# Performance work log

Hardware: AMD Instinct MI355X
Metric: run time of the kernel (lower is better)

## Reference

```python
import jax, jax.numpy as jnp
import numpy as np

DIM = 512
HEADS = 8
SCALE = (DIM // HEADS) ** -0.5  # 0.125
B, H, W = 1, 64, 64  # square spatial grid required by torch matmul broadcasting


def setup_inputs() -> dict:
    key = jax.random.key(0)
    ks = jax.random.split(key, 7)
    s = DIM ** -0.5
    return {
        "x": jax.random.normal(ks[0], (B, H, W, DIM), dtype=jnp.float32),
        "mask": 0,  # sentinel for None (mask must be None in the original)
        "Wq": jax.random.normal(ks[1], (DIM, DIM), dtype=jnp.float32) * s,
        "bq": jax.random.normal(ks[2], (DIM,), dtype=jnp.float32) * 0.01,
        "Wk": jax.random.normal(ks[3], (DIM, DIM), dtype=jnp.float32) * s,
        "bk": jax.random.normal(ks[4], (DIM,), dtype=jnp.float32) * 0.01,
        "Wv": jax.random.normal(ks[5], (DIM, DIM), dtype=jnp.float32) * s,
        "bv": jax.random.normal(ks[6], (DIM,), dtype=jnp.float32) * 0.01,
    }


def reference(x, mask, Wq, bq, Wk, bk, Wv, bv):
    # Linear projections (nn.Linear: x @ W.T + b)
    q = jnp.einsum('bhwc,oc->bhwo', x, Wq) + bq
    k = jnp.einsum('bhwc,oc->bhwo', x, Wk) + bk
    v = jnp.einsum('bhwc,oc->bhwo', x, Wv) + bv
    # Faithful to torch.einsum('bhwc,bpqd->bhwpq', q, k): c and d are each
    # summed independently => outer product of channel-sums. [b,h,w,p,q]
    weights = jnp.einsum('bhwc,bpqd->bhwpq', q, k)
    # dropout is identity in eval mode; then scale and softmax over last axis
    weights = jax.nn.softmax(weights * SCALE, axis=-1)
    # torch matmul broadcasting: [b,h,w,p,q] @ [b,p,q,d] -> [b,h,w,p,d]
    attn = jnp.matmul(weights, v)
    return attn
```

## Files before the change

### kernel.cpp

```cpp
#include <hip/hip_runtime.h>

typedef _Float16 half8 __attribute__((ext_vector_type(8)));
typedef float f32x4 __attribute__((ext_vector_type(4)));
typedef float float4_t __attribute__((ext_vector_type(4)));
typedef unsigned int uint32x2 __attribute__((ext_vector_type(2)));

#define DIM 512
#define S 64
#define NROW 4096
#define LDSW 88

__global__ void colsum2_kernel(const float* __restrict__ Wq, const float* __restrict__ bq,
                               const float* __restrict__ Wk, const float* __restrict__ bk,
                               float* __restrict__ wsumq, float* __restrict__ wsumk) {
    int sel = blockIdx.x >> 5;
    int b = blockIdx.x & 31;
    const float* W = sel ? Wk : Wq;
    const float* bias = sel ? bk : bq;
    float* wsum = sel ? wsumk : wsumq;
    int t = threadIdx.x;
    int c0 = t, c1 = t + 256;
    float s0 = 0.f, s1 = 0.f;
    const float* Wr = W + (size_t)b * 16 * DIM;
#pragma unroll
    for (int o = 0; o < 16; ++o) {
        s0 += Wr[o * DIM + c0];
        s1 += Wr[o * DIM + c1];
    }
    atomicAdd(&wsum[c0], s0);
    atomicAdd(&wsum[c1], s1);
    if (b == 0) {
        float bs = bias[c0] + bias[c1];
#pragma unroll
        for (int off = 32; off >= 1; off >>= 1) bs += __shfl_xor(bs, off);
        if ((t & 63) == 0) atomicAdd(&wsum[512], bs);
    }
}

__global__ void rowdot_kernel(const float* __restrict__ X,
                              const float* __restrict__ wqsum,
                              const float* __restrict__ wksum,
                              float* __restrict__ a_arr,
                              float* __restrict__ ks_arr) {
    int wave = threadIdx.x >> 6;
    int lane = threadIdx.x & 63;
    int row = blockIdx.x * 4 + wave;
    const float4_t* xr = (const float4_t*)(X + (size_t)row * DIM) + lane * 2;
    const float4_t* wq = (const float4_t*)wqsum + lane * 2;
    const float4_t* wk = (const float4_t*)wksum + lane * 2;
    float4_t x0 = xr[0], x1 = xr[1];
    float4_t q0 = wq[0], q1 = wq[1];
    float4_t k0 = wk[0], k1 = wk[1];
    float sq = 0.f, sk = 0.f;
#pragma unroll
    for (int i = 0; i < 4; i++) {
        sq += x0[i] * q0[i] + x1[i] * q1[i];
        sk += x0[i] * k0[i] + x1[i] * k1[i];
    }
#pragma unroll
    for (int off = 32; off >= 1; off >>= 1) {
        sq += __shfl_xor(sq, off);
        sk += __shfl_xor(sk, off);
    }
    if (lane == 0) {
        a_arr[row]  = (sq + wqsum[DIM]) * 0.125f;
        ks_arr[row] = sk + wksum[DIM];
    }
}

__global__ void vt_gemm_kernel(const float* __restrict__ X,
                               const float* __restrict__ Wv,
                               const float* __restrict__ bv,
                               _Float16* __restrict__ Vs) {
    int mb = blockIdx.x;
    int cb = blockIdx.y;
    int wv_ = threadIdx.x >> 6;
    int lane = threadIdx.x & 63;
    int lr = lane & 15;
    int lg = lane >> 4;
    int row0 = mb * 16;
    int col0 = cb * 256 + wv_ * 64;

    f32x4 acc[4];
#pragma unroll
    for (int n = 0; n < 4; n++) acc[n] = (f32x4){0.f, 0.f, 0.f, 0.f};

    for (int kk = 0; kk < 16; ++kk) {
        int kbase = kk * 32 + lg * 8;
        const float4_t* pa = (const float4_t*)(X + (size_t)(row0 + lr) * DIM + kbase);
        float4_t x0 = pa[0], x1 = pa[1];
        half8 a;
#pragma unroll
        for (int i = 0; i < 4; i++) { a[i] = (_Float16)x0[i]; a[i + 4] = (_Float16)x1[i]; }
#pragma unroll
        for (int n = 0; n < 4; n++) {
            const float4_t* pb = (const float4_t*)(Wv + (size_t)(col0 + n * 16 + lr) * DIM + kbase);
            float4_t b0 = pb[0], b1 = pb[1];
            half8 hb;
#pragma unroll
            for (int i = 0; i < 4; i++) { hb[i] = (_Float16)b0[i]; hb[i + 4] = (_Float16)b1[i]; }
            acc[n] = __builtin_amdgcn_mfma_f32_16x16x32_f16(a, hb, acc[n], 0, 0, 0);
        }
    }
    int w   = mb >> 2;
    int s_  = (mb & 3) >> 1;
    int lg2 = ((mb & 3) * 2 + (lg >> 1)) & 3;
    int e0  = (lg & 1) * 4;
#pragma unroll
    for (int n = 0; n < 4; n++) {
        int d = col0 + n * 16 + lr;
        int dt = d >> 4;
        float bvc = bv[d];
        _Float16 tmp[4];
#pragma unroll
        for (int r = 0; r < 4; r++) tmp[r] = (_Float16)(acc[n][r] + bvc);
        int idx8 = (((w * 32 + dt) * 2 + s_) * 4 + lg2) * 16 + lr;
        __builtin_nontemporal_store(*(uint32x2*)tmp, (uint32x2*)(Vs + (size_t)idx8 * 8 + e0));
    }
}

__global__ __launch_bounds__(256) void attn_main_kernel(
        const float* __restrict__ a_arr,
        const float* __restrict__ ks_arr,
        const _Float16* __restrict__ Vs,
        float* __restrict__ out) {
    __shared__ _Float16 Wsm[64 * LDSW];
    __shared__ float Osm[64 * 128];
    int hw = blockIdx.x;
    int w = hw & 63;
    int t = threadIdx.x;
    int wv_ = t >> 6, lane = t & 63;
    int lr = lane & 15, lg = lane >> 4;

    float a = a_arr[hw];

    {
        int p = t >> 2, c = t & 3;
        const float4_t* kp = (const float4_t*)(ks_arr + p * 64 + c * 16);
        float4_t k0 = kp[0], k1 = kp[1], k2 = kp[2], k3 = kp[3];
        float L[16];
#pragma unroll
        for (int i = 0; i < 4; i++) {
            L[i] = a * k0[i]; L[4 + i] = a * k1[i];
            L[8 + i] = a * k2[i]; L[12 + i] = a * k3[i];
        }
        float m = L[0];
#pragma unroll
        for (int i = 1; i < 16; i++) m = fmaxf(m, L[i]);
        m = fmaxf(m, __shfl_xor(m, 1));
        m = fmaxf(m, __shfl_xor(m, 2));
        float e[16];
        float sum = 0.f;
#pragma unroll
        for (int i = 0; i < 16; i++) { e[i] = __expf(L[i] - m); sum += e[i]; }
        sum += __shfl_xor(sum, 1);
        sum += __shfl_xor(sum, 2);
        float r = 1.0f / sum;
        half8 h0, h1;
#pragma unroll
        for (int i = 0; i < 8; i++) {
            h0[i] = (_Float16)(e[i] * r);
            h1[i] = (_Float16)(e[8 + i] * r);
        }
        *(half8*)&Wsm[p * LDSW + c * 16]     = h0;
        *(half8*)&Wsm[p * LDSW + c * 16 + 8] = h1;
    }
    __syncthreads();

    half8 wfr[4][2];
#pragma unroll
    for (int pt = 0; pt < 4; ++pt)
#pragma unroll
        for (int s_ = 0; s_ < 2; ++s_)
            wfr[pt][s_] = *(const half8*)&Wsm[(pt * 16 + lr) * LDSW + s_ * 32 + lg * 8];

    const half8* Vg = (const half8*)Vs;
    char* outb = (char*)(out + (size_t)hw * (64 * DIM));

    for (int j2 = 0; j2 < 4; ++j2) {
        int dt0 = j2 * 8 + wv_ * 2;
        half8 v00 = Vg[((w * 32 + dt0) * 2 + 0) * 64 + lane];
        half8 v01 = Vg[((w * 32 + dt0) * 2 + 1) * 64 + lane];
        half8 v10 = Vg[((w * 32 + dt0 + 1) * 2 + 0) * 64 + lane];
        half8 v11 = Vg[((w * 32 + dt0 + 1) * 2 + 1) * 64 + lane];
        f32x4 acc[2][4];
#pragma unroll
        for (int c = 0; c < 2; ++c)
#pragma unroll
            for (int pt = 0; pt < 4; ++pt) acc[c][pt] = (f32x4){0.f, 0.f, 0.f, 0.f};
#pragma unroll
        for (int pt = 0; pt < 4; ++pt) {
            acc[0][pt] = __builtin_amdgcn_mfma_f32_16x16x32_f16(v00, wfr[pt][0], acc[0][pt], 0, 0, 0);
            acc[0][pt] = __builtin_amdgcn_mfma_f32_16x16x32_f16(v01, wfr[pt][1], acc[0][pt], 0, 0, 0);
            acc[1][pt] = __builtin_amdgcn_mfma_f32_16x16x32_f16(v10, wfr[pt][0], acc[1][pt], 0, 0, 0);
            acc[1][pt] = __builtin_amdgcn_mfma_f32_16x16x32_f16(v11, wfr[pt][1], acc[1][pt], 0, 0, 0);
        }
        __syncthreads();
#pragma unroll
        for (int c = 0; c < 2; ++c)
#pragma unroll
            for (int pt = 0; pt < 4; ++pt) {
                int p = pt * 16 + lr;
                int addr = p * 512 + (wv_ * 32 + c * 16 + lg * 4) * 4;
                addr ^= (p & 7) << 4;
                *(f32x4*)((char*)Osm + addr) = acc[c][pt];
            }
        __syncthreads();
#pragma unroll
        for (int i = 0; i < 8; ++i) {
            int f = i * 4096 + t * 16;
            int row = f >> 9;
            int rb = f ^ ((row & 7) << 4);
            f32x4 val = *(const f32x4*)((const char*)Osm + rb);
            __builtin_nontemporal_store(val, (f32x4*)(outb + (size_t)row * 2048 + j2 * 512 + (f & 511)));
        }
    }
}

extern "C" void kernel_launch(void* const* d_in, const int* in_sizes, int n_in,
                              void* d_out, int out_size, void* d_ws, size_t ws_size,
                              hipStream_t stream) {
    const float* x  = (const float*)d_in[0];
    const float* Wq = (const float*)d_in[2];
    const float* bq = (const float*)d_in[3];
    const float* Wk = (const float*)d_in[4];
    const float* bk = (const float*)d_in[5];
    const float* Wv = (const float*)d_in[6];
    const float* bv = (const float*)d_in[7];
    float* out = (float*)d_out;
    char* ws = (char*)d_ws;

    _Float16* Vs  = (_Float16*)ws;
    float* a_arr  = (float*)(ws + 4194304);
    float* ks_arr = (float*)(ws + 4210688);
    float* wqsum  = (float*)(ws + 4227072);
    float* wksum  = (float*)(ws + 4229184);

    hipMemsetAsync(ws + 4227072, 0, 4224, stream);
    colsum2_kernel<<<64, 256, 0, stream>>>(Wq, bq, Wk, bk, wqsum, wksum);
    rowdot_kernel<<<1024, 256, 0, stream>>>(x, wqsum, wksum, a_arr, ks_arr);
    vt_gemm_kernel<<<dim3(256, 2), 256, 0, stream>>>(x, Wv, bv, Vs);
    attn_main_kernel<<<4096, 256, 0, stream>>>(a_arr, ks_arr, Vs, out);
}
```

Measured before the change: 147.8 us.

## Merge rowdot and V GEMM launches, prefetch V tiles, use lighter LDS barriers

Folds the rowdot and V-projection GEMM kernels into one launch whose block index picks the role, removing one kernel launch and its gap. In the attention kernel, the V fragments for the next output chunk are loaded one iteration ahead, so global loads overlap the MFMA and store phases. The j2 loop is fully unrolled. __syncthreads is replaced by a barrier that waits only on LDS counters, so outstanding global loads are not drained at each barrier. This costs more registers per thread and relies on correct manual waitcnt handling.

```diff
diff --git a/kernel.cpp b/kernel.cpp
--- a/kernel.cpp
+++ b/kernel.cpp
@@ -9,6 +9,12 @@
 #define S 64
 #define NROW 4096
 #define LDSW 88
+
+__device__ __forceinline__ void bar_lds() {
+    asm volatile("s_waitcnt lgkmcnt(0)" ::: "memory");
+    __builtin_amdgcn_s_barrier();
+    asm volatile("" ::: "memory");
+}
 
 __global__ void colsum2_kernel(const float* __restrict__ Wq, const float* __restrict__ bq,
                                const float* __restrict__ Wk, const float* __restrict__ bk,
@@ -37,43 +43,45 @@
     }
 }
 
-__global__ void rowdot_kernel(const float* __restrict__ X,
-                              const float* __restrict__ wqsum,
-                              const float* __restrict__ wksum,
-                              float* __restrict__ a_arr,
-                              float* __restrict__ ks_arr) {
-    int wave = threadIdx.x >> 6;
-    int lane = threadIdx.x & 63;
-    int row = blockIdx.x * 4 + wave;
-    const float4_t* xr = (const float4_t*)(X + (size_t)row * DIM) + lane * 2;
-    const float4_t* wq = (const float4_t*)wqsum + lane * 2;
-    const float4_t* wk = (const float4_t*)wksum + lane * 2;
-    float4_t x0 = xr[0], x1 = xr[1];
-    float4_t q0 = wq[0], q1 = wq[1];
-    float4_t k0 = wk[0], k1 = wk[1];
-    float sq = 0.f, sk = 0.f;
-#pragma unroll
-    for (int i = 0; i < 4; i++) {
-        sq += x0[i] * q0[i] + x1[i] * q1[i];
-        sk += x0[i] * k0[i] + x1[i] * k1[i];
-    }
-#pragma unroll
-    for (int off = 32; off >= 1; off >>= 1) {
-        sq += __shfl_xor(sq, off);
-        sk += __shfl_xor(sk, off);
-    }
-    if (lane == 0) {
-        a_arr[row]  = (sq + wqsum[DIM]) * 0.125f;
-        ks_arr[row] = sk + wksum[DIM];
-    }
-}
-
-__global__ void vt_gemm_kernel(const float* __restrict__ X,
-                               const float* __restrict__ Wv,
-                               const float* __restrict__ bv,
-                               _Float16* __restrict__ Vs) {
-    int mb = blockIdx.x;
-    int cb = blockIdx.y;
+__global__ void rowdot_vt_kernel(const float* __restrict__ X,
+                                 const float* __restrict__ wqsum,
+                                 const float* __restrict__ wksum,
+                                 float* __restrict__ a_arr,
+                                 float* __restrict__ ks_arr,
+                                 const float* __restrict__ Wv,
+                                 const float* __restrict__ bv,
+                                 _Float16* __restrict__ Vs) {
+    int bid = blockIdx.x;
+    if (bid < 1024) {
+        int wave = threadIdx.x >> 6;
+        int lane = threadIdx.x & 63;
+        int row = bid * 4 + wave;
+        const float4_t* xr = (const float4_t*)(X + (size_t)row * DIM) + lane * 2;
+        const float4_t* wq = (const float4_t*)wqsum + lane * 2;
+        const float4_t* wk = (const float4_t*)wksum + lane * 2;
+        float4_t x0 = xr[0], x1 = xr[1];
+        float4_t q0 = wq[0], q1 = wq[1];
+        float4_t k0 = wk[0], k1 = wk[1];
+        float sq = 0.f, sk = 0.f;
+#pragma unroll
+        for (int i = 0; i < 4; i++) {
+            sq += x0[i] * q0[i] + x1[i] * q1[i];
+            sk += x0[i] * k0[i] + x1[i] * k1[i];
+        }
+#pragma unroll
+        for (int off = 32; off >= 1; off >>= 1) {
+            sq += __shfl_xor(sq, off);
+            sk += __shfl_xor(sk, off);
+        }
+        if (lane == 0) {
+            a_arr[row]  = (sq + wqsum[DIM]) * 0.125f;
+            ks_arr[row] = sk + wksum[DIM];
+        }
+        return;
+    }
+    int b2 = bid - 1024;
+    int mb = b2 & 255;
+    int cb = b2 >> 8;
     int wv_ = threadIdx.x >> 6;
     int lane = threadIdx.x & 63;
     int lr = lane & 15;
@@ -132,6 +140,14 @@
     int wv_ = t >> 6, lane = t & 63;
     int lr = lane & 15, lg = lane >> 4;
 
+    const half8* Vg = (const half8*)Vs;
+
+    int dtb = wv_ * 2;
+    half8 vc0 = Vg[((w * 32 + dtb) * 2 + 0) * 64 + lane];
+    half8 vc1 = Vg[((w * 32 + dtb) * 2 + 1) * 64 + lane];
+    half8 vc2 = Vg[((w * 32 + dtb + 1) * 2 + 0) * 64 + lane];
+    half8 vc3 = Vg[((w * 32 + dtb + 1) * 2 + 1) * 64 + lane];
+
     float a = a_arr[hw];
 
     {
@@ -165,7 +181,7 @@
         *(half8*)&Wsm[p * LDSW + c * 16]     = h0;
         *(half8*)&Wsm[p * LDSW + c * 16 + 8] = h1;
     }
-    __syncthreads();
+    bar_lds();
 
     half8 wfr[4][2];
 #pragma unroll
@@ -174,15 +190,18 @@
         for (int s_ = 0; s_ < 2; ++s_)
             wfr[pt][s_] = *(const half8*)&Wsm[(pt * 16 + lr) * LDSW + s_ * 32 + lg * 8];
 
-    const half8* Vg = (const half8*)Vs;
     char* outb = (char*)(out + (size_t)hw * (64 * DIM));
 
+#pragma unroll
     for (int j2 = 0; j2 < 4; ++j2) {
-        int dt0 = j2 * 8 + wv_ * 2;
-        half8 v00 = Vg[((w * 32 + dt0) * 2 + 0) * 64 + lane];
-        half8 v01 = Vg[((w * 32 + dt0) * 2 + 1) * 64 + lane];
-        half8 v10 = Vg[((w * 32 + dt0 + 1) * 2 + 0) * 64 + lane];
-        half8 v11 = Vg[((w * 32 + dt0 + 1) * 2 + 1) * 64 + lane];
+        half8 vn0, vn1, vn2, vn3;
+        if (j2 < 3) {
+            int dt0 = (j2 + 1) * 8 + dtb;
+            vn0 = Vg[((w * 32 + dt0) * 2 + 0) * 64 + lane];
+            vn1 = Vg[((w * 32 + dt0) * 2 + 1) * 64 + lane];
+            vn2 = Vg[((w * 32 + dt0 + 1) * 2 + 0) * 64 + lane];
+            vn3 = Vg[((w * 32 + dt0 + 1) * 2 + 1) * 64 + lane];
+        }
         f32x4 acc[2][4];
 #pragma unroll
         for (int c = 0; c < 2; ++c)
@@ -190,12 +209,12 @@
             for (int pt = 0; pt < 4; ++pt) acc[c][pt] = (f32x4){0.f, 0.f, 0.f, 0.f};
 #pragma unroll
         for (int pt = 0; pt < 4; ++pt) {
-            acc[0][pt] = __builtin_amdgcn_mfma_f32_16x16x32_f16(v00, wfr[pt][0], acc[0][pt], 0, 0, 0);
-            acc[0][pt] = __builtin_amdgcn_mfma_f32_16x16x32_f16(v01, wfr[pt][1], acc[0][pt], 0, 0, 0);
-            acc[1][pt] = __builtin_amdgcn_mfma_f32_16x16x32_f16(v10, wfr[pt][0], acc[1][pt], 0, 0, 0);
-            acc[1][pt] = __builtin_amdgcn_mfma_f32_16x16x32_f16(v11, wfr[pt][1], acc[1][pt], 0, 0, 0);
-        }
-        __syncthreads();
+            acc[0][pt] = __builtin_amdgcn_mfma_f32_16x16x32_f16(vc0, wfr[pt][0], acc[0][pt], 0, 0, 0);
+            acc[0][pt] = __builtin_amdgcn_mfma_f32_16x16x32_f16(vc1, wfr[pt][1], acc[0][pt], 0, 0, 0);
+            acc[1][pt] = __builtin_amdgcn_mfma_f32_16x16x32_f16(vc2, wfr[pt][0], acc[1][pt], 0, 0, 0);
+            acc[1][pt] = __builtin_amdgcn_mfma_f32_16x16x32_f16(vc3, wfr[pt][1], acc[1][pt], 0, 0, 0);
+        }
+        bar_lds();
 #pragma unroll
         for (int c = 0; c < 2; ++c)
 #pragma unroll
@@ -205,7 +224,7 @@
                 addr ^= (p & 7) << 4;
                 *(f32x4*)((char*)Osm + addr) = acc[c][pt];
             }
-        __syncthreads();
+        bar_lds();
 #pragma unroll
         for (int i = 0; i < 8; ++i) {
             int f = i * 4096 + t * 16;
@@ -214,6 +233,7 @@
             f32x4 val = *(const f32x4*)((const char*)Osm + rb);
             __builtin_nontemporal_store(val, (f32x4*)(outb + (size_t)row * 2048 + j2 * 512 + (f & 511)));
         }
+        vc0 = vn0; vc1 = vn1; vc2 = vn2; vc3 = vn3;
     }
 }
 
@@ -238,7 +258,6 @@
 
     hipMemsetAsync(ws + 4227072, 0, 4224, stream);
     colsum2_kernel<<<64, 256, 0, stream>>>(Wq, bq, Wk, bk, wqsum, wksum);
-    rowdot_kernel<<<1024, 256, 0, stream>>>(x, wqsum, wksum, a_arr, ks_arr);
-    vt_gemm_kernel<<<dim3(256, 2), 256, 0, stream>>>(x, Wv, bv, Vs);
+    rowdot_vt_kernel<<<1536, 256, 0, stream>>>(x, wqsum, wksum, a_arr, ks_arr, Wv, bv, Vs);
     attn_main_kernel<<<4096, 256, 0, stream>>>(a_arr, ks_arr, Vs, out);
 }
```

After: 147.7 us. No clear change (-0.0%).
